# Kernel tuning notes

Hardware: AMD Instinct MI355X
Metric: run time of the kernel (lower is better)

Reference implementation:

```python
import jax, jax.numpy as jnp
import numpy as np

SIGMA = 0.5          # cone height of the distance field
B, NV, NF, MAXC = 32, 6890, 13776, 8
NC = NF * MAXC       # padded number of collision pair slots


def setup_inputs() -> dict:
    key = jax.random.key(0)
    ks = jax.random.split(key, 8)
    return {
        "pose": jax.random.normal(ks[0], (B, 72), jnp.float32),
        "joints": jax.random.normal(ks[1], (B, 24, 3), jnp.float32),
        "points": jax.random.normal(ks[2], (B, 118, 3), jnp.float32),
        "keypoints": jax.random.normal(ks[3], (B, 118, 3), jnp.float32),
        "vertices": jax.random.normal(ks[4], (B, NV, 3), jnp.float32),
        "weight": jnp.ones((1,), jnp.float32),
        "faces": jax.random.randint(ks[5], (NF, 3), 0, NV, dtype=jnp.int32),
        "collision_idxs": jax.random.randint(ks[6], (B, NC, 2), 0, NF, dtype=jnp.int32),
    }


def _cone_point2plane(cone_tris, query_tris):
    """Conic distance-field penetration (point2plane), vectorized over pairs.
    cone_tris/query_tris: [B, C, 3 verts, 3 xyz]. Returns [B, C]."""
    c = cone_tris.mean(axis=-2)                              # centroid [B,C,3]
    e1 = cone_tris[..., 1, :] - cone_tris[..., 0, :]
    e2 = cone_tris[..., 2, :] - cone_tris[..., 0, :]
    n = jnp.cross(e1, e2)
    n = n / (jnp.linalg.norm(n, axis=-1, keepdims=True) + 1e-8)
    d = query_tris - c[..., None, :]                         # [B,C,3,3]
    h = jnp.einsum('bcvk,bck->bcv', d, n)                    # signed plane dist
    r = jnp.linalg.norm(d, axis=-1)                          # dist to centroid
    phi = jnp.maximum(SIGMA - r, 0.0)                        # linear cone field
    pen = jnp.where(h < 0, phi * h * h, 0.0)                 # penetrating verts only
    return pen.sum(axis=-1)


def reference(pose, joints, points, keypoints, vertices, weight, faces, collision_idxs):
    # polygons = verts.view(-1,3)[faces_idx]  ->  per-batch face gather
    tris = jnp.take(vertices, faces, axis=1)                 # [B,NF,3,3]
    recv_idx = collision_idxs[..., 0]
    intr_idx = collision_idxs[..., 1]
    valid = recv_idx >= 0                                    # -1 padding slots

    def gather(idx):
        idx = jnp.maximum(idx, 0)[:, :, None, None]
        return jnp.take_along_axis(tris, idx, axis=1)        # [B,NC,3,3]

    recv = gather(recv_idx)
    intr = gather(intr_idx)
    # symmetric penetration: intruder verts in receiver's field and vice versa
    pen = _cone_point2plane(recv, intr) + _cone_point2plane(intr, recv)
    loss = jnp.where(valid, pen, 0.0).sum() / B
    return loss * weight[0]
```

## Files before the change

kernel.cpp:

```cpp
#include <hip/hip_runtime.h>

#define SIGMA 0.5f
#define BB 32
#define NVV 6890
#define NFF 13776
#define MAXC 8
#define NCC (NFF * MAXC)

#define REC_HALFS 16
#define REC_BYTES ((size_t)BB * NFF * REC_HALFS * sizeof(_Float16))

#define PAIRS_PER_BLOCK 512
#define SLOTS2 ((NCC + PAIRS_PER_BLOCK - 1) / PAIRS_PER_BLOCK)
#define NPART (BB * SLOTS2)

typedef int v4i __attribute__((ext_vector_type(4)));

union RecU {
    uint4    u[2];
    _Float16 h[16];
};

__device__ __forceinline__ float3 loadv3(const float* __restrict__ p) {
    return make_float3(p[0], p[1], p[2]);
}

__global__ __launch_bounds__(256) void face_kernel(
    const float* __restrict__ vertices,
    const int*   __restrict__ faces,
    uint4*       __restrict__ rec)
{
    const int i = blockIdx.x * blockDim.x + threadIdx.x;
    if (i >= BB * NFF) return;
    const int b = i / NFF;
    const int f = i - b * NFF;

    const float* vb = vertices + (size_t)b * (NVV * 3);
    const int i0 = faces[f * 3 + 0];
    const int i1 = faces[f * 3 + 1];
    const int i2 = faces[f * 3 + 2];
    float3 v0 = loadv3(vb + (size_t)i0 * 3);
    float3 v1 = loadv3(vb + (size_t)i1 * 3);
    float3 v2 = loadv3(vb + (size_t)i2 * 3);

    const float third = 1.0f / 3.0f;
    float cx = (v0.x + v1.x + v2.x) * third;
    float cy = (v0.y + v1.y + v2.y) * third;
    float cz = (v0.z + v1.z + v2.z) * third;

    float e1x = v1.x - v0.x, e1y = v1.y - v0.y, e1z = v1.z - v0.z;
    float e2x = v2.x - v0.x, e2y = v2.y - v0.y, e2z = v2.z - v0.z;
    float nx = e1y * e2z - e1z * e2y;
    float ny = e1z * e2x - e1x * e2z;
    float nz = e1x * e2y - e1y * e2x;
    float inv = 1.0f / (sqrtf(nx * nx + ny * ny + nz * nz) + 1e-8f);
    nx *= inv; ny *= inv; nz *= inv;

    RecU r;
    r.h[0]  = (_Float16)cx;   r.h[1]  = (_Float16)cy;   r.h[2]  = (_Float16)cz;
    r.h[3]  = (_Float16)nx;   r.h[4]  = (_Float16)ny;   r.h[5]  = (_Float16)nz;
    r.h[6]  = (_Float16)v0.x; r.h[7]  = (_Float16)v0.y; r.h[8]  = (_Float16)v0.z;
    r.h[9]  = (_Float16)v1.x; r.h[10] = (_Float16)v1.y; r.h[11] = (_Float16)v1.z;
    r.h[12] = (_Float16)v2.x; r.h[13] = (_Float16)v2.y; r.h[14] = (_Float16)v2.z;
    r.h[15] = (_Float16)0.0f;

    uint4* dst = rec + (size_t)i * 2;
    dst[0] = r.u[0];
    dst[1] = r.u[1];
}

__device__ __forceinline__ float penSide(float cx, float cy, float cz,
                                         float nx, float ny, float nz,
                                         const float* q) {
    float pen = 0.0f;
#pragma unroll
    for (int v = 0; v < 3; ++v) {
        float dx = q[3 * v + 0] - cx;
        float dy = q[3 * v + 1] - cy;
        float dz = q[3 * v + 2] - cz;
        float h = dx * nx + dy * ny + dz * nz;
        float r = sqrtf(dx * dx + dy * dy + dz * dz);
        float phi = fmaxf(SIGMA - r, 0.0f);
        pen += (h < 0.0f) ? phi * h * h : 0.0f;
    }
    return pen;
}

__device__ __forceinline__ float recPen(const uint4* __restrict__ rec,
                                        int b, int f0, int f1) {
    if (f0 < 0) return 0.0f;
    const int g1 = f1 < 0 ? 0 : f1;
    const uint4* ra = rec + ((size_t)b * NFF + f0) * 2;
    const uint4* rb = rec + ((size_t)b * NFF + g1) * 2;
    RecU A, B;
    A.u[0] = ra[0]; A.u[1] = ra[1];
    B.u[0] = rb[0]; B.u[1] = rb[1];

    float qa[9], qb[9];
#pragma unroll
    for (int k = 0; k < 9; ++k) { qa[k] = (float)A.h[6 + k]; qb[k] = (float)B.h[6 + k]; }

    float pen = penSide((float)A.h[0], (float)A.h[1], (float)A.h[2],
                        (float)A.h[3], (float)A.h[4], (float)A.h[5], qb);
    pen      += penSide((float)B.h[0], (float)B.h[1], (float)B.h[2],
                        (float)B.h[3], (float)B.h[4], (float)B.h[5], qa);
    return pen;
}

__global__ __launch_bounds__(256) void pair_kernel(
    const uint4* __restrict__ rec,
    const int*   __restrict__ cidx,
    float*       __restrict__ partials)
{
    const int b    = blockIdx.x;
    const int slot = blockIdx.y;
    const int base = slot * PAIRS_PER_BLOCK + threadIdx.x * 2;
    float pen = 0.0f;

    if (base < NCC) {
        const v4i* c4 = (const v4i*)(cidx + (size_t)b * NCC * 2) + (slot * 256 + threadIdx.x);
        v4i pr = __builtin_nontemporal_load(c4);
        pen = recPen(rec, b, pr.x, pr.y) + recPen(rec, b, pr.z, pr.w);
    }

#pragma unroll
    for (int off = 32; off > 0; off >>= 1)
        pen += __shfl_down(pen, off, 64);

    __shared__ float smem[4];
    const int lane = threadIdx.x & 63;
    const int wv   = threadIdx.x >> 6;
    if (lane == 0) smem[wv] = pen;
    __syncthreads();
    if (threadIdx.x == 0)
        partials[(size_t)b * SLOTS2 + slot] = smem[0] + smem[1] + smem[2] + smem[3];
}

__global__ __launch_bounds__(1024) void reduce_kernel(
    const float* __restrict__ partials,
    const float* __restrict__ weight,
    float*       __restrict__ out)
{
    float s = 0.0f;
    for (int i = threadIdx.x; i < NPART; i += 1024)
        s += partials[i];
#pragma unroll
    for (int off = 32; off > 0; off >>= 1)
        s += __shfl_down(s, off, 64);

    __shared__ float smem[16];
    const int lane = threadIdx.x & 63;
    const int wv   = threadIdx.x >> 6;
    if (lane == 0) smem[wv] = s;
    __syncthreads();
    if (threadIdx.x == 0) {
        float t = 0.0f;
#pragma unroll
        for (int w = 0; w < 16; ++w) t += smem[w];
        out[0] = t * weight[0] * (1.0f / (float)BB);
    }
}

__global__ void init_kernel(float* __restrict__ accum) { accum[0] = 0.0f; }

__device__ __forceinline__ float conePen(float3 a0, float3 a1, float3 a2,
                                         float3 q0, float3 q1, float3 q2) {
    const float third = 1.0f / 3.0f;
    float cx = (a0.x + a1.x + a2.x) * third;
    float cy = (a0.y + a1.y + a2.y) * third;
    float cz = (a0.z + a1.z + a2.z) * third;
    float e1x = a1.x - a0.x, e1y = a1.y - a0.y, e1z = a1.z - a0.z;
    float e2x = a2.x - a0.x, e2y = a2.y - a0.y, e2z = a2.z - a0.z;
    float nx = e1y * e2z - e1z * e2y;
    float ny = e1z * e2x - e1x * e2z;
    float nz = e1x * e2y - e1y * e2x;
    float inv = 1.0f / (sqrtf(nx * nx + ny * ny + nz * nz) + 1e-8f);
    nx *= inv; ny *= inv; nz *= inv;
    float3 q[3] = {q0, q1, q2};
    float pen = 0.0f;
#pragma unroll
    for (int v = 0; v < 3; ++v) {
        float dx = q[v].x - cx, dy = q[v].y - cy, dz = q[v].z - cz;
        float h = dx * nx + dy * ny + dz * nz;
        float r = sqrtf(dx * dx + dy * dy + dz * dz);
        float phi = fmaxf(SIGMA - r, 0.0f);
        pen += (h < 0.0f) ? phi * h * h : 0.0f;
    }
    return pen;
}

__global__ __launch_bounds__(256) void pen_direct(
    const float* __restrict__ vertices, const int* __restrict__ faces,
    const int2* __restrict__ cidx, float* __restrict__ accum)
{
    const int i = blockIdx.x * blockDim.x + threadIdx.x;
    float pen = 0.0f;
    if (i < BB * NCC) {
        const int b = i / NCC;
        const int2 pr = cidx[i];
        if (pr.x >= 0) {
            const int f0 = pr.x;
            const int f1 = pr.y < 0 ? 0 : pr.y;
            const float* vb = vertices + (size_t)b * (NVV * 3);
            float3 a0 = loadv3(vb + (size_t)faces[f0*3+0] * 3);
            float3 a1 = loadv3(vb + (size_t)faces[f0*3+1] * 3);
            float3 a2 = loadv3(vb + (size_t)faces[f0*3+2] * 3);
            float3 b0 = loadv3(vb + (size_t)faces[f1*3+0] * 3);
            float3 b1 = loadv3(vb + (size_t)faces[f1*3+1] * 3);
            float3 b2 = loadv3(vb + (size_t)faces[f1*3+2] * 3);
            pen = conePen(a0,a1,a2,b0,b1,b2) + conePen(b0,b1,b2,a0,a1,a2);
        }
    }
#pragma unroll
    for (int off = 32; off > 0; off >>= 1)
        pen += __shfl_down(pen, off, 64);
    __shared__ float smem[4];
    const int lane = threadIdx.x & 63;
    const int wv   = threadIdx.x >> 6;
    if (lane == 0) smem[wv] = pen;
    __syncthreads();
    if (threadIdx.x == 0)
        atomicAdd(accum, smem[0] + smem[1] + smem[2] + smem[3]);
}

__global__ void fin_kernel(const float* __restrict__ accum,
                           const float* __restrict__ weight,
                           float* __restrict__ out)
{
    out[0] = accum[0] * weight[0] * (1.0f / (float)BB);
}

extern "C" void kernel_launch(void* const* d_in, const int* in_sizes, int n_in,
                              void* d_out, int out_size, void* d_ws, size_t ws_size,
                              hipStream_t stream) {
    const float* vertices = (const float*)d_in[4];
    const float* weight   = (const float*)d_in[5];
    const int*   faces    = (const int*)d_in[6];
    const int*   cidx     = (const int*)d_in[7];
    float* out = (float*)d_out;

    if (ws_size >= REC_BYTES + NPART * sizeof(float) + 256) {
        uint4* rec      = (uint4*)d_ws;
        float* partials = (float*)((char*)d_ws + REC_BYTES);

        const int totalFaces = BB * NFF;
        face_kernel<<<dim3((totalFaces + 255) / 256), dim3(256), 0, stream>>>(
            vertices, faces, rec);
        pair_kernel<<<dim3(BB, SLOTS2), dim3(256), 0, stream>>>(rec, cidx, partials);
        reduce_kernel<<<dim3(1), dim3(1024), 0, stream>>>(partials, weight, out);
    } else {
        float* accum = (float*)d_ws;
        const int totalPairs = BB * NCC;
        init_kernel<<<dim3(1), dim3(1), 0, stream>>>(accum);
        pen_direct<<<dim3((totalPairs + 255) / 256), dim3(256), 0, stream>>>(
            vertices, faces, (const int2*)cidx, accum);
        fin_kernel<<<dim3(1), dim3(1), 0, stream>>>(accum, weight, out);
    }
}
```

Before: 131.1 us.

## Fuse face and pair kernels with per-batch vertex mesh staged in LDS

Replaces the separate face-record kernel and pair kernel with one fused kernel. Each block loads one batch's full vertex array (about 83 KB fp32) and bit-packed face indices (about 69 KB) into shared memory, then evaluates its slice of collision pairs with LDS gathers and recomputes centroids and normals per pair. This removes the fp16 face-record write and read through global memory along with one launch, but it recomputes face geometry for every pair, reloads the mesh in each of 8 blocks per batch, and allows only one 1024-thread block per CU because of the LDS footprint. With only 256 blocks in total, the GPU may be underfilled.

```diff
diff --git a/kernel.cpp b/kernel.cpp
--- a/kernel.cpp
+++ b/kernel.cpp
@@ -7,161 +7,16 @@
 #define MAXC 8
 #define NCC (NFF * MAXC)
 
-#define REC_HALFS 16
-#define REC_BYTES ((size_t)BB * NFF * REC_HALFS * sizeof(_Float16))
-
-#define PAIRS_PER_BLOCK 512
-#define SLOTS2 ((NCC + PAIRS_PER_BLOCK - 1) / PAIRS_PER_BLOCK)
-#define NPART (BB * SLOTS2)
+#define SLOTS 8
+#define PAIRS_PER_SLOT (NCC / SLOTS)
+#define THREADS 1024
+#define NBLOCK (BB * SLOTS)
 
 typedef int v4i __attribute__((ext_vector_type(4)));
-
-union RecU {
-    uint4    u[2];
-    _Float16 h[16];
-};
 
 __device__ __forceinline__ float3 loadv3(const float* __restrict__ p) {
     return make_float3(p[0], p[1], p[2]);
 }
-
-__global__ __launch_bounds__(256) void face_kernel(
-    const float* __restrict__ vertices,
-    const int*   __restrict__ faces,
-    uint4*       __restrict__ rec)
-{
-    const int i = blockIdx.x * blockDim.x + threadIdx.x;
-    if (i >= BB * NFF) return;
-    const int b = i / NFF;
-    const int f = i - b * NFF;
-
-    const float* vb = vertices + (size_t)b * (NVV * 3);
-    const int i0 = faces[f * 3 + 0];
-    const int i1 = faces[f * 3 + 1];
-    const int i2 = faces[f * 3 + 2];
-    float3 v0 = loadv3(vb + (size_t)i0 * 3);
-    float3 v1 = loadv3(vb + (size_t)i1 * 3);
-    float3 v2 = loadv3(vb + (size_t)i2 * 3);
-
-    const float third = 1.0f / 3.0f;
-    float cx = (v0.x + v1.x + v2.x) * third;
-    float cy = (v0.y + v1.y + v2.y) * third;
-    float cz = (v0.z + v1.z + v2.z) * third;
-
-    float e1x = v1.x - v0.x, e1y = v1.y - v0.y, e1z = v1.z - v0.z;
-    float e2x = v2.x - v0.x, e2y = v2.y - v0.y, e2z = v2.z - v0.z;
-    float nx = e1y * e2z - e1z * e2y;
-    float ny = e1z * e2x - e1x * e2z;
-    float nz = e1x * e2y - e1y * e2x;
-    float inv = 1.0f / (sqrtf(nx * nx + ny * ny + nz * nz) + 1e-8f);
-    nx *= inv; ny *= inv; nz *= inv;
-
-    RecU r;
-    r.h[0]  = (_Float16)cx;   r.h[1]  = (_Float16)cy;   r.h[2]  = (_Float16)cz;
-    r.h[3]  = (_Float16)nx;   r.h[4]  = (_Float16)ny;   r.h[5]  = (_Float16)nz;
-    r.h[6]  = (_Float16)v0.x; r.h[7]  = (_Float16)v0.y; r.h[8]  = (_Float16)v0.z;
-    r.h[9]  = (_Float16)v1.x; r.h[10] = (_Float16)v1.y; r.h[11] = (_Float16)v1.z;
-    r.h[12] = (_Float16)v2.x; r.h[13] = (_Float16)v2.y; r.h[14] = (_Float16)v2.z;
-    r.h[15] = (_Float16)0.0f;
-
-    uint4* dst = rec + (size_t)i * 2;
-    dst[0] = r.u[0];
-    dst[1] = r.u[1];
-}
-
-__device__ __forceinline__ float penSide(float cx, float cy, float cz,
-                                         float nx, float ny, float nz,
-                                         const float* q) {
-    float pen = 0.0f;
-#pragma unroll
-    for (int v = 0; v < 3; ++v) {
-        float dx = q[3 * v + 0] - cx;
-        float dy = q[3 * v + 1] - cy;
-        float dz = q[3 * v + 2] - cz;
-        float h = dx * nx + dy * ny + dz * nz;
-        float r = sqrtf(dx * dx + dy * dy + dz * dz);
-        float phi = fmaxf(SIGMA - r, 0.0f);
-        pen += (h < 0.0f) ? phi * h * h : 0.0f;
-    }
-    return pen;
-}
-
-__device__ __forceinline__ float recPen(const uint4* __restrict__ rec,
-                                        int b, int f0, int f1) {
-    if (f0 < 0) return 0.0f;
-    const int g1 = f1 < 0 ? 0 : f1;
-    const uint4* ra = rec + ((size_t)b * NFF + f0) * 2;
-    const uint4* rb = rec + ((size_t)b * NFF + g1) * 2;
-    RecU A, B;
-    A.u[0] = ra[0]; A.u[1] = ra[1];
-    B.u[0] = rb[0]; B.u[1] = rb[1];
-
-    float qa[9], qb[9];
-#pragma unroll
-    for (int k = 0; k < 9; ++k) { qa[k] = (float)A.h[6 + k]; qb[k] = (float)B.h[6 + k]; }
-
-    float pen = penSide((float)A.h[0], (float)A.h[1], (float)A.h[2],
-                        (float)A.h[3], (float)A.h[4], (float)A.h[5], qb);
-    pen      += penSide((float)B.h[0], (float)B.h[1], (float)B.h[2],
-                        (float)B.h[3], (float)B.h[4], (float)B.h[5], qa);
-    return pen;
-}
-
-__global__ __launch_bounds__(256) void pair_kernel(
-    const uint4* __restrict__ rec,
-    const int*   __restrict__ cidx,
-    float*       __restrict__ partials)
-{
-    const int b    = blockIdx.x;
-    const int slot = blockIdx.y;
-    const int base = slot * PAIRS_PER_BLOCK + threadIdx.x * 2;
-    float pen = 0.0f;
-
-    if (base < NCC) {
-        const v4i* c4 = (const v4i*)(cidx + (size_t)b * NCC * 2) + (slot * 256 + threadIdx.x);
-        v4i pr = __builtin_nontemporal_load(c4);
-        pen = recPen(rec, b, pr.x, pr.y) + recPen(rec, b, pr.z, pr.w);
-    }
-
-#pragma unroll
-    for (int off = 32; off > 0; off >>= 1)
-        pen += __shfl_down(pen, off, 64);
-
-    __shared__ float smem[4];
-    const int lane = threadIdx.x & 63;
-    const int wv   = threadIdx.x >> 6;
-    if (lane == 0) smem[wv] = pen;
-    __syncthreads();
-    if (threadIdx.x == 0)
-        partials[(size_t)b * SLOTS2 + slot] = smem[0] + smem[1] + smem[2] + smem[3];
-}
-
-__global__ __launch_bounds__(1024) void reduce_kernel(
-    const float* __restrict__ partials,
-    const float* __restrict__ weight,
-    float*       __restrict__ out)
-{
-    float s = 0.0f;
-    for (int i = threadIdx.x; i < NPART; i += 1024)
-        s += partials[i];
-#pragma unroll
-    for (int off = 32; off > 0; off >>= 1)
-        s += __shfl_down(s, off, 64);
-
-    __shared__ float smem[16];
-    const int lane = threadIdx.x & 63;
-    const int wv   = threadIdx.x >> 6;
-    if (lane == 0) smem[wv] = s;
-    __syncthreads();
-    if (threadIdx.x == 0) {
-        float t = 0.0f;
-#pragma unroll
-        for (int w = 0; w < 16; ++w) t += smem[w];
-        out[0] = t * weight[0] * (1.0f / (float)BB);
-    }
-}
-
-__global__ void init_kernel(float* __restrict__ accum) { accum[0] = 0.0f; }
 
 __device__ __forceinline__ float conePen(float3 a0, float3 a1, float3 a2,
                                          float3 q0, float3 q1, float3 q2) {
@@ -188,6 +43,97 @@
     }
     return pen;
 }
+
+__device__ __forceinline__ float3 ldsVert(const float* __restrict__ sv, int v) {
+    return make_float3(sv[3 * v + 0], sv[3 * v + 1], sv[3 * v + 2]);
+}
+
+__device__ __forceinline__ float pairPen(const float* __restrict__ sv,
+                                         const unsigned int* __restrict__ fw,
+                                         const unsigned char* __restrict__ fb,
+                                         int r, int it) {
+    if (r < 0) return 0.0f;
+    const int g = it < 0 ? 0 : it;
+    unsigned int wa = fw[r];
+    unsigned int wb = fw[g];
+    int a0 = wa & 8191, a1 = (wa >> 13) & 8191, a2 = (int)(wa >> 26) | ((int)fb[r] << 6);
+    int b0 = wb & 8191, b1 = (wb >> 13) & 8191, b2 = (int)(wb >> 26) | ((int)fb[g] << 6);
+    float3 A0 = ldsVert(sv, a0), A1 = ldsVert(sv, a1), A2 = ldsVert(sv, a2);
+    float3 B0 = ldsVert(sv, b0), B1 = ldsVert(sv, b1), B2 = ldsVert(sv, b2);
+    return conePen(A0, A1, A2, B0, B1, B2) + conePen(B0, B1, B2, A0, A1, A2);
+}
+
+__global__ __launch_bounds__(THREADS) void fused_kernel(
+    const float* __restrict__ vertices,
+    const int*   __restrict__ faces,
+    const int*   __restrict__ cidx,
+    float*       __restrict__ partials)
+{
+    __shared__ float         s_v[NVV * 3];
+    __shared__ unsigned int  s_fw[NFF];
+    __shared__ unsigned char s_fb[NFF];
+    __shared__ float         s_red[16];
+
+    const int b   = blockIdx.x;
+    const int sl  = blockIdx.y;
+    const int tid = threadIdx.x;
+
+    const float* vb = vertices + (size_t)b * (NVV * 3);
+    for (int i = tid; i < NVV * 3; i += THREADS)
+        s_v[i] = vb[i];
+
+    for (int f = tid; f < NFF; f += THREADS) {
+        int i0 = faces[3 * f + 0];
+        int i1 = faces[3 * f + 1];
+        int i2 = faces[3 * f + 2];
+        s_fw[f] = (unsigned int)i0 | ((unsigned int)i1 << 13)
+                | ((unsigned int)(i2 & 63) << 26);
+        s_fb[f] = (unsigned char)(i2 >> 6);
+    }
+    __syncthreads();
+
+    float pen = 0.0f;
+    const v4i* c4 = (const v4i*)(cidx + ((size_t)b * NCC + (size_t)sl * PAIRS_PER_SLOT) * 2);
+    for (int q = tid; 2 * q < PAIRS_PER_SLOT; q += THREADS) {
+        v4i pr = __builtin_nontemporal_load(c4 + q);
+        pen += pairPen(s_v, s_fw, s_fb, pr.x, pr.y);
+        pen += pairPen(s_v, s_fw, s_fb, pr.z, pr.w);
+    }
+
+#pragma unroll
+    for (int off = 32; off > 0; off >>= 1)
+        pen += __shfl_down(pen, off, 64);
+    const int lane = tid & 63;
+    const int wv   = tid >> 6;
+    if (lane == 0) s_red[wv] = pen;
+    __syncthreads();
+    if (tid == 0) {
+        float t = 0.0f;
+#pragma unroll
+        for (int w = 0; w < 16; ++w) t += s_red[w];
+        partials[b * SLOTS + sl] = t;
+    }
+}
+
+__global__ __launch_bounds__(256) void fin2_kernel(
+    const float* __restrict__ partials,
+    const float* __restrict__ weight,
+    float*       __restrict__ out)
+{
+    float s = partials[threadIdx.x];
+#pragma unroll
+    for (int off = 32; off > 0; off >>= 1)
+        s += __shfl_down(s, off, 64);
+    __shared__ float smem[4];
+    const int lane = threadIdx.x & 63;
+    const int wv   = threadIdx.x >> 6;
+    if (lane == 0) smem[wv] = s;
+    __syncthreads();
+    if (threadIdx.x == 0)
+        out[0] = (smem[0] + smem[1] + smem[2] + smem[3]) * weight[0] * (1.0f / (float)BB);
+}
+
+__global__ void init_kernel(float* __restrict__ accum) { accum[0] = 0.0f; }
 
 __global__ __launch_bounds__(256) void pen_direct(
     const float* __restrict__ vertices, const int* __restrict__ faces,
@@ -239,15 +185,11 @@
     const int*   cidx     = (const int*)d_in[7];
     float* out = (float*)d_out;
 
-    if (ws_size >= REC_BYTES + NPART * sizeof(float) + 256) {
-        uint4* rec      = (uint4*)d_ws;
-        float* partials = (float*)((char*)d_ws + REC_BYTES);
-
-        const int totalFaces = BB * NFF;
-        face_kernel<<<dim3((totalFaces + 255) / 256), dim3(256), 0, stream>>>(
-            vertices, faces, rec);
-        pair_kernel<<<dim3(BB, SLOTS2), dim3(256), 0, stream>>>(rec, cidx, partials);
-        reduce_kernel<<<dim3(1), dim3(1024), 0, stream>>>(partials, weight, out);
+    if (ws_size >= NBLOCK * sizeof(float)) {
+        float* partials = (float*)d_ws;
+        fused_kernel<<<dim3(BB, SLOTS), dim3(THREADS), 0, stream>>>(
+            vertices, faces, cidx, partials);
+        fin2_kernel<<<dim3(1), dim3(256), 0, stream>>>(partials, weight, out);
     } else {
         float* accum = (float*)d_ws;
         const int totalPairs = BB * NCC;
```

After: 123.7 us. 5.6% less time.
